# Kernel optimization log

Measured on AMD Instinct MI355X. Metric: run time of the kernel, lower is better.

Reference implementation:

```python
import jax, jax.numpy as jnp
import numpy as np

L = 1024  # seq_len


def setup_inputs() -> dict:
    key = jax.random.key(0)
    ks = jax.random.split(key, 9)
    B = 4
    x = jax.random.uniform(ks[0], (B, L, L), dtype=jnp.float32)          # scores from pre_model
    M = (jax.random.uniform(ks[1], (B, L, L)) < 0.5).astype(jnp.float32)  # pairing-constraint mask
    M = M * M.transpose(0, 2, 1)  # symmetric binary mask
    return {
        "x": x,
        "M": M,
        "s": jnp.float32(0.5),
        "w": jax.random.uniform(ks[2], (1,), dtype=jnp.float32),
        "rho_p": jax.random.uniform(ks[3], (L, L), dtype=jnp.float32),
        "alpha": jnp.float32(0.005),
        "belt": jnp.float32(0.05),
        "lr_alpha": jnp.float32(0.99),
        "lr_belt": jnp.float32(0.99),
        "steps": 16,
    }


def _T_A(A_hat, M):
    # symmetrize then mask
    return (A_hat + A_hat.transpose(0, 2, 1)) * 0.5 * M


def reference(x, M, s, w, rho_p, alpha, belt, lr_alpha, lr_belt, steps):
    scores = x                      # pre_model output, [B, L, L]
    U = scores - s
    A_hat0 = scores
    A0 = _T_A(A_hat0, M)
    Lm0 = w * jax.nn.relu(jnp.sum(A0, axis=-1) - 1.0)   # [B, L] (w broadcasts)

    def step(carry, t):
        Lm, A, A_hat = carry
        # G = U/2 - Lm * sign(rowsum(A) - 1), broadcast over last dim
        row = jnp.sum(A, axis=-1) - 1.0                  # [B, L]
        G = U * 0.5 - (Lm * jnp.sign(row))[:, :, None]   # [B, L, L]
        at = alpha * jnp.power(lr_alpha, t)
        A_hat = A_hat + at * A_hat * M * (G + G.transpose(0, 2, 1))
        A_hat = jax.nn.relu(jnp.abs(A_hat) - rho_p * at)  # soft threshold
        A_hat = 1.0 - jax.nn.relu(1.0 - A_hat)            # clip above at 1
        A = _T_A(A_hat, M)
        Lm = Lm + belt * jnp.power(lr_belt, t) * jax.nn.relu(jnp.sum(A, axis=-1) - 1.0)
        return (Lm, A, A_hat), None

    ts = jnp.arange(steps, dtype=jnp.float32)
    (Lm, A, A_hat), _ = jax.lax.scan(step, (Lm0, A0, A_hat0), ts)
    return A
```

## Files before the change

### kernel.cpp

```cpp
#include <hip/hip_runtime.h>
#include <cstddef>
#include <math.h>

static constexpr int L = 1024;
static constexpr int B = 4;
static constexpr int NSTEPS = 16;
static constexpr int NTILE = 16;
static constexpr int NPAIR = NTILE * (NTILE + 1) / 2;
static constexpr int BL = B * L;
static constexpr int NBLK = 256;
static constexpr int NBANK = 4;
static constexpr int NGRP = 16;
static constexpr int GBLK = NBLK / NGRP;

static constexpr size_t AH_OFF  = 0;
static constexpr size_t US_OFF  = (size_t)B * L * L;
static constexpr size_t CP_OFF  = 2 * (size_t)B * L * L;
static constexpr size_t RP0_OFF = CP_OFF + (size_t)B * 256 * L;
static constexpr size_t CP0_OFF = RP0_OFF + (size_t)B * 16 * L;
static constexpr size_t R_OFF   = CP0_OFF + (size_t)B * 16 * L;
static constexpr size_t LM_OFF  = R_OFF + (size_t)B * L;
static constexpr size_t CC_OFF  = LM_OFF + (size_t)B * L;
static constexpr size_t SC_OFF  = CC_OFF + (size_t)B * L;
static constexpr size_t RS_OFF  = SC_OFF + 64;
static constexpr size_t CS_OFF  = RS_OFF + (size_t)(NSTEPS - 1) * BL;
static constexpr size_t CS_U64  = (size_t)(NSTEPS - 1) * NBANK * BL;
static constexpr size_t BAR_OFF = CS_OFF + 2 * CS_U64;
static constexpr size_t NZERO_U64 = CS_U64 + 520;

__global__ __launch_bounds__(256) void init_kernel(
    const float* __restrict__ x, const float* __restrict__ M,
    const float* __restrict__ sp,
    float* __restrict__ ah, float* __restrict__ us,
    float* __restrict__ Rpart, float* __restrict__ Cpart0,
    unsigned long long* __restrict__ Cs)
{
    __shared__ float lt[64][65];
    __shared__ float cpw[4][64];
    const int bid  = blockIdx.x;
    {
        const size_t gid = (size_t)bid * 256 + threadIdx.x;
        if (gid < NZERO_U64) Cs[gid] = 0ull;
    }
    const int chunk = bid & 7;
    const int rest  = bid >> 3;
    const int b  = rest >> 5;
    const int ti = (chunk << 1) | ((rest >> 4) & 1);
    const int tj = rest & 15;
    const int t  = threadIdx.x;
    const int w  = t >> 6;
    const int r  = t >> 4;
    const int c4 = (t & 15) << 2;
    const float s = sp[0];
    const float* xb = x + (size_t)b * L * L;

#pragma unroll
    for (int it = 0; it < 4; ++it) {
        int rr = r + 16 * it;
        float4 v = *(const float4*)(xb + (size_t)(tj * 64 + rr) * L + ti * 64 + c4);
        lt[rr][c4+0] = v.x; lt[rr][c4+1] = v.y; lt[rr][c4+2] = v.z; lt[rr][c4+3] = v.w;
    }
    __syncthreads();

    float cs0 = 0.f, cs1 = 0.f, cs2 = 0.f, cs3 = 0.f;
#pragma unroll
    for (int it = 0; it < 4; ++it) {
        int rr = r + 16 * it;
        int gi = ti * 64 + rr;
        size_t off = (size_t)b * L * L + (size_t)gi * L + tj * 64 + c4;
        float4 xv = *(const float4*)(x + off);
        float4 mv = *(const float4*)(M + off);
        *(float4*)(us + off) = make_float4(0.5f*(xv.x + lt[c4+0][rr]) - s,
                                           0.5f*(xv.y + lt[c4+1][rr]) - s,
                                           0.5f*(xv.z + lt[c4+2][rr]) - s,
                                           0.5f*(xv.w + lt[c4+3][rr]) - s);
        float a0 = xv.x*mv.x, a1 = xv.y*mv.y, a2 = xv.z*mv.z, a3 = xv.w*mv.w;
        *(float4*)(ah + off) = make_float4(a0, a1, a2, a3);
        float rs = (a0 + a1) + (a2 + a3);
        rs += __shfl_xor(rs, 1); rs += __shfl_xor(rs, 2);
        rs += __shfl_xor(rs, 4); rs += __shfl_xor(rs, 8);
        if ((t & 15) == 0) Rpart[((size_t)(b * 16 + tj)) * L + gi] = rs;
        cs0 += a0; cs1 += a1; cs2 += a2; cs3 += a3;
    }
    cs0 += __shfl_xor(cs0, 16); cs0 += __shfl_xor(cs0, 32);
    cs1 += __shfl_xor(cs1, 16); cs1 += __shfl_xor(cs1, 32);
    cs2 += __shfl_xor(cs2, 16); cs2 += __shfl_xor(cs2, 32);
    cs3 += __shfl_xor(cs3, 16); cs3 += __shfl_xor(cs3, 32);
    if ((t & 63) < 16) {
        int c0 = (t & 63) << 2;
        cpw[w][c0+0] = cs0; cpw[w][c0+1] = cs1; cpw[w][c0+2] = cs2; cpw[w][c0+3] = cs3;
    }
    __syncthreads();
    if (t < 64)
        Cpart0[((size_t)(b * 16 + ti)) * L + tj * 64 + t] =
            (cpw[0][t] + cpw[1][t]) + (cpw[2][t] + cpw[3][t]);
}

__global__ __launch_bounds__(256) void lminit_kernel(
    const float* __restrict__ wp,
    const float* __restrict__ alphap, const float* __restrict__ beltp,
    const float* __restrict__ lrap,  const float* __restrict__ lrbp,
    const float* __restrict__ Rpart, const float* __restrict__ Cpart0,
    float* __restrict__ Lm, float* __restrict__ cc, float* __restrict__ sc)
{
    const int bid = blockIdx.x;
    const int t   = threadIdx.x;
    if (bid == 0 && t < NSTEPS) {
        sc[t]          = alphap[0] * powf(lrap[0], (float)t);
        sc[NSTEPS + t] = beltp[0]  * powf(lrbp[0], (float)t);
    }
    const int b   = bid >> 2;
    const int i   = ((bid & 3) << 8) + t;
    float R0 = 0.f, C0 = 0.f;
#pragma unroll
    for (int k = 0; k < 16; ++k) {
        R0 += Rpart[((size_t)(b * 16 + k)) * L + i];
        C0 += Cpart0[((size_t)(b * 16 + k)) * L + i];
    }
    float rowv = 0.5f * (R0 + C0) - 1.0f;
    float rl = fmaxf(rowv, 0.f);
    float lm = wp[0] * rl;
    Lm[b * L + i] = lm;
    float sg = (rowv > 0.f) ? 1.f : ((rowv < 0.f) ? -1.f : 0.f);
    cc[b * L + i] = lm * sg;
}

__device__ __forceinline__ float step_elem(float a, float u, float rho,
                                           float ci, float cj, float at) {
    float g = u - ci - cj;
    float v = a * (1.f + at * g);
    v = fmaxf(fabsf(v) - rho * at, 0.f);
    return fminf(v, 1.f);
}

__global__ __launch_bounds__(1024, 4) void steps_kernel(
    const float* __restrict__ rho, const float* __restrict__ sc,
    float* __restrict__ ah, const float* __restrict__ us,
    const float* __restrict__ Lm0, const float* __restrict__ cc0,
    float* __restrict__ Rs, unsigned long long* __restrict__ Cs,
    unsigned int* __restrict__ bar)
{
    __shared__ float cc_lds[1024];
    __shared__ float lm_lds[1024];
    __shared__ float cp[8][1024];

    const int t    = threadIdx.x;
    const int w    = t >> 6;
    const int l    = t & 63;
    const int bid  = blockIdx.x;
    const int xcd  = bid & 7;
    const int idx  = bid >> 3;
    const int b    = idx >> 3;
    const int slab = (xcd << 3) | (idx & 7);
    const int row  = (slab << 4) | w;
    const int bank = xcd & 3;
    const int grp  = bid >> 4;
    const size_t rowoff = (size_t)b * L * L + (size_t)row * L;
    const float* rrow = rho + (size_t)row * L;
    unsigned int* gctr = bar + grp * 64;
    unsigned int* root = bar + NGRP * 64;

    cc_lds[t] = cc0[b * L + t];
    lm_lds[t] = Lm0[b * L + t];

    float4 a4[4], u4[4];
#pragma unroll
    for (int k = 0; k < 4; ++k) {
        const size_t off = rowoff + (k << 8) + (l << 2);
        a4[k] = *(const float4*)(ah + off);
        u4[k] = *(const float4*)(us + off);
    }
    __syncthreads();

    for (int p = 0; p < NSTEPS; ++p) {
        const float at = sc[p];
        const float ci = cc_lds[row];
        float rs = 0.f;
#pragma unroll
        for (int k = 0; k < 4; ++k) {
            float4 h  = *(const float4*)(rrow + (k << 8) + (l << 2));
            float4 c4 = *(const float4*)&cc_lds[(k << 8) + (l << 2)];
            a4[k].x = step_elem(a4[k].x, u4[k].x, h.x, ci, c4.x, at);
            a4[k].y = step_elem(a4[k].y, u4[k].y, h.y, ci, c4.y, at);
            a4[k].z = step_elem(a4[k].z, u4[k].z, h.z, ci, c4.z, at);
            a4[k].w = step_elem(a4[k].w, u4[k].w, h.w, ci, c4.w, at);
            rs += (a4[k].x + a4[k].y) + (a4[k].z + a4[k].w);
        }
        if (p == NSTEPS - 1) break;

        rs += __shfl_xor(rs, 1);  rs += __shfl_xor(rs, 2);  rs += __shfl_xor(rs, 4);
        rs += __shfl_xor(rs, 8);  rs += __shfl_xor(rs, 16); rs += __shfl_xor(rs, 32);
        if (l == 0)
            __hip_atomic_store(&Rs[(size_t)p * BL + b * L + row], rs,
                               __ATOMIC_RELAXED, __HIP_MEMORY_SCOPE_AGENT);

        if (w >= 8) {
#pragma unroll
            for (int k = 0; k < 4; ++k)
                *(float4*)&cp[w - 8][(k << 8) + (l << 2)] = a4[k];
        }
        __syncthreads();
        if (w < 8) {
#pragma unroll
            for (int k = 0; k < 4; ++k) {
                float4* q = (float4*)&cp[w][(k << 8) + (l << 2)];
                float4 v = *q;
                v.x += a4[k].x; v.y += a4[k].y; v.z += a4[k].z; v.w += a4[k].w;
                *q = v;
            }
        }
        __syncthreads();
        float csum = 0.f;
#pragma unroll
        for (int j = 0; j < 8; ++j) csum += cp[j][t];
        atomicAdd(Cs + ((size_t)(p * NBANK + bank)) * BL + b * L + t,
                  (unsigned long long)((double)csum * 4294967296.0));

        __syncthreads();
        if (t == 0) {
            unsigned old = __hip_atomic_fetch_add(gctr, 1u, __ATOMIC_ACQ_REL,
                                                  __HIP_MEMORY_SCOPE_AGENT);
            if (old == (unsigned)(p * GBLK + GBLK - 1))
                __hip_atomic_fetch_add(root, 1u, __ATOMIC_ACQ_REL,
                                       __HIP_MEMORY_SCOPE_AGENT);
            const unsigned target = (unsigned)(p + 1) * (unsigned)NGRP;
            while (__hip_atomic_load(root, __ATOMIC_RELAXED,
                                     __HIP_MEMORY_SCOPE_AGENT) < target)
                __builtin_amdgcn_s_sleep(4);
            (void)__hip_atomic_load(root, __ATOMIC_ACQUIRE,
                                    __HIP_MEMORY_SCOPE_AGENT);
        }
        __syncthreads();

        {
            const size_t cbase = (size_t)p * NBANK * BL + b * L + t;
            unsigned long long craw = 0ull;
#pragma unroll
            for (int q = 0; q < NBANK; ++q)
                craw += __hip_atomic_load(&Cs[cbase + (size_t)q * BL],
                                          __ATOMIC_RELAXED, __HIP_MEMORY_SCOPE_AGENT);
            float Rv = __hip_atomic_load(
                &Rs[(size_t)p * BL + b * L + t],
                __ATOMIC_RELAXED, __HIP_MEMORY_SCOPE_AGENT);
            float Cv = (float)((double)(long long)craw * (1.0 / 4294967296.0));
            float rowv = 0.5f * (Rv + Cv) - 1.0f;
            float lm = lm_lds[t] + sc[NSTEPS + p] * fmaxf(rowv, 0.f);
            lm_lds[t] = lm;
            cc_lds[t] = lm * ((rowv > 0.f) ? 1.f : ((rowv < 0.f) ? -1.f : 0.f));
        }
        __syncthreads();
    }

#pragma unroll
    for (int k = 0; k < 4; ++k)
        *(float4*)(ah + rowoff + (k << 8) + (l << 2)) = a4[k];
}

template <bool DO_SUMS>
__global__ __launch_bounds__(512) void update_kernel(
    const float* __restrict__ rho, const float* __restrict__ sc,
    float* __restrict__ ah, const float* __restrict__ us,
    const float* __restrict__ cc,
    float* __restrict__ R, float* __restrict__ Cpart, int p)
{
    __shared__ float cp[8][1024];
    const int bid   = blockIdx.x;
    const int chunk = bid & 7;
    const int rest  = bid >> 3;
    const int b     = rest >> 4;
    const int slab  = (chunk << 4) | (rest & 15);
    const int t    = threadIdx.x;
    const int w    = t >> 6;
    const int l    = t & 63;
    const int row  = (slab << 3) + w;
    const size_t rowoff = (size_t)b * L * L + (size_t)row * L;
    const float at = sc[p];
    const float* ccb = cc + b * L;

    float4 cj[4];
#pragma unroll
    for (int k = 0; k < 4; ++k)
        cj[k] = *(const float4*)(ccb + k * 256 + l * 4);
    const float ci = ccb[row];

    float4 a4[4], u4[4], h4[4];
#pragma unroll
    for (int k = 0; k < 4; ++k) {
        const size_t off = rowoff + k * 256 + l * 4;
        a4[k] = *(const float4*)(ah + off);
        u4[k] = *(const float4*)(us + off);
        h4[k] = *(const float4*)(rho + (size_t)row * L + k * 256 + l * 4);
    }
#pragma unroll
    for (int k = 0; k < 4; ++k) {
        a4[k].x = step_elem(a4[k].x, u4[k].x, h4[k].x, ci, cj[k].x, at);
        a4[k].y = step_elem(a4[k].y, u4[k].y, h4[k].y, ci, cj[k].y, at);
        a4[k].z = step_elem(a4[k].z, u4[k].z, h4[k].z, ci, cj[k].z, at);
        a4[k].w = step_elem(a4[k].w, u4[k].w, h4[k].w, ci, cj[k].w, at);
        *(float4*)(ah + rowoff + k * 256 + l * 4) = a4[k];
    }

    if (DO_SUMS) {
        float rs = 0.f;
#pragma unroll
        for (int k = 0; k < 4; ++k)
            rs += (a4[k].x + a4[k].y) + (a4[k].z + a4[k].w);
        rs += __shfl_xor(rs, 1);  rs += __shfl_xor(rs, 2);  rs += __shfl_xor(rs, 4);
        rs += __shfl_xor(rs, 8);  rs += __shfl_xor(rs, 16); rs += __shfl_xor(rs, 32);
        if (l == 0) R[b * L + row] = rs;

#pragma unroll
        for (int k = 0; k < 4; ++k)
            *(float4*)&cp[w][k * 256 + l * 4] = a4[k];
        __syncthreads();
        const int c0 = t * 2;
        float2 acc = make_float2(0.f, 0.f);
#pragma unroll
        for (int j = 0; j < 8; ++j) {
            float2 v = *(float2*)&cp[j][c0];
            acc.x += v.x; acc.y += v.y;
        }
        *(float2*)(Cpart + ((size_t)(b * 128 + slab)) * L + c0) = acc;
    }
}

__global__ __launch_bounds__(1024) void lmreduce_kernel(
    const float* __restrict__ sc,
    const float* __restrict__ Cpart, const float* __restrict__ R,
    float* __restrict__ Lm, float* __restrict__ cc, int p)
{
    __shared__ float red[16][64];
    const int bid = blockIdx.x;
    const int b   = bid >> 4;
    const int c0  = (bid & 15) << 6;
    const int t   = threadIdx.x;
    const int w   = t >> 6;
    const int l   = t & 63;
    const int c   = c0 + l;

    const float* base = Cpart + (size_t)b * 128 * L + c;
    float v = 0.f;
#pragma unroll
    for (int k = w * 8; k < w * 8 + 8; ++k)
        v += base[(size_t)k * L];
    red[w][l] = v;
    __syncthreads();

    if (w == 0) {
        float total = 0.f;
#pragma unroll
        for (int j = 0; j < 16; ++j) total += red[j][l];
        float rowv = 0.5f * (R[b * L + c] + total) - 1.0f;
        float rl = fmaxf(rowv, 0.f);
        float lm = Lm[b * L + c] + sc[NSTEPS + p] * rl;
        Lm[b * L + c] = lm;
        float sg = (rowv > 0.f) ? 1.f : ((rowv < 0.f) ? -1.f : 0.f);
        cc[b * L + c] = lm * sg;
    }
}

__device__ __forceinline__ void decode_pair(int p, int& ti, int& tj) {
    int t = 0;
    while (p >= NTILE - t) { p -= NTILE - t; ++t; }
    ti = t; tj = t + p;
}

__global__ __launch_bounds__(256) void final_kernel(
    const float* __restrict__ ah, float* __restrict__ out)
{
    __shared__ float la[64][65];
    __shared__ float lb[64][65];
    const int task = blockIdx.x;
    const int b = task / NPAIR;
    int ti, tj; decode_pair(task % NPAIR, ti, tj);
    const int t  = threadIdx.x;
    const int r0 = t >> 4;
    const int c0 = (t & 15) << 2;
    const float* ahb = ah  + (size_t)b * L * L;
    float* ob        = out + (size_t)b * L * L;

    for (int it = 0; it < 4; ++it) {
        int r = r0 + 16 * it;
        float4 va = *(const float4*)(ahb + (size_t)(ti * 64 + r) * L + tj * 64 + c0);
        la[r][c0+0] = va.x; la[r][c0+1] = va.y; la[r][c0+2] = va.z; la[r][c0+3] = va.w;
        if (ti != tj) {
            float4 vb = *(const float4*)(ahb + (size_t)(tj * 64 + r) * L + ti * 64 + c0);
            lb[r][c0+0] = vb.x; lb[r][c0+1] = vb.y; lb[r][c0+2] = vb.z; lb[r][c0+3] = vb.w;
        }
    }
    __syncthreads();

    for (int it = 0; it < 4; ++it) {
        int r = r0 + 16 * it;
        size_t off = (size_t)(ti * 64 + r) * L + tj * 64 + c0;
        float tb0, tb1, tb2, tb3;
        if (ti == tj) { tb0 = la[c0+0][r]; tb1 = la[c0+1][r]; tb2 = la[c0+2][r]; tb3 = la[c0+3][r]; }
        else          { tb0 = lb[c0+0][r]; tb1 = lb[c0+1][r]; tb2 = lb[c0+2][r]; tb3 = lb[c0+3][r]; }
        *(float4*)(ob + off) = make_float4(0.5f*(la[r][c0+0]+tb0), 0.5f*(la[r][c0+1]+tb1),
                                           0.5f*(la[r][c0+2]+tb2), 0.5f*(la[r][c0+3]+tb3));
    }
    if (ti != tj) {
        for (int it = 0; it < 4; ++it) {
            int r = r0 + 16 * it;
            size_t off = (size_t)(tj * 64 + r) * L + ti * 64 + c0;
            *(float4*)(ob + off) = make_float4(0.5f*(lb[r][c0+0]+la[c0+0][r]),
                                               0.5f*(lb[r][c0+1]+la[c0+1][r]),
                                               0.5f*(lb[r][c0+2]+la[c0+2][r]),
                                               0.5f*(lb[r][c0+3]+la[c0+3][r]));
        }
    }
}

extern "C" void kernel_launch(void* const* d_in, const int* in_sizes, int n_in,
                              void* d_out, int out_size, void* d_ws, size_t ws_size,
                              hipStream_t stream) {
    const float* x     = (const float*)d_in[0];
    const float* M     = (const float*)d_in[1];
    const float* s     = (const float*)d_in[2];
    const float* w     = (const float*)d_in[3];
    const float* rho   = (const float*)d_in[4];
    const float* alpha = (const float*)d_in[5];
    const float* belt  = (const float*)d_in[6];
    const float* lra   = (const float*)d_in[7];
    const float* lrb   = (const float*)d_in[8];
    float* out = (float*)d_out;

    float* ws     = (float*)d_ws;
    float* ah     = ws + AH_OFF;
    float* us     = ws + US_OFF;
    float* Cpart  = ws + CP_OFF;
    float* Rpart  = ws + RP0_OFF;
    float* Cpart0 = ws + CP0_OFF;
    float* R      = ws + R_OFF;
    float* Lm     = ws + LM_OFF;
    float* cc     = ws + CC_OFF;
    float* sc     = ws + SC_OFF;
    float* Rs     = ws + RS_OFF;
    unsigned long long* Cs = (unsigned long long*)(ws + CS_OFF);
    unsigned int* bar      = (unsigned int*)(ws + BAR_OFF);

    init_kernel<<<dim3(1024), dim3(256), 0, stream>>>(x, M, s, ah, us, Rpart, Cpart0, Cs);
    lminit_kernel<<<dim3(16), dim3(256), 0, stream>>>(
        w, alpha, belt, lra, lrb, Rpart, Cpart0, Lm, cc, sc);

    {
        const float* rho_ = rho; const float* sc_ = sc;
        float* ah_ = ah; const float* us_ = us;
        const float* Lm_ = Lm; const float* cc_ = cc;
        float* Rs_ = Rs; unsigned long long* Cs_ = Cs;
        unsigned int* bar_ = bar;
        void* args[] = { &rho_, &sc_, &ah_, &us_, &Lm_, &cc_, &Rs_, &Cs_, &bar_ };
        hipError_t err = hipLaunchCooperativeKernel(
            (void*)steps_kernel, dim3(NBLK), dim3(1024), args, 0, stream);
        if (err != hipSuccess) {
            for (int p = 0; p < NSTEPS; ++p) {
                if (p < NSTEPS - 1) {
                    update_kernel<true><<<dim3(512), dim3(512), 0, stream>>>(
                        rho, sc, ah, us, cc, R, Cpart, p);
                    lmreduce_kernel<<<dim3(64), dim3(1024), 0, stream>>>(
                        sc, Cpart, R, Lm, cc, p);
                } else {
                    update_kernel<false><<<dim3(512), dim3(512), 0, stream>>>(
                        rho, sc, ah, us, cc, R, Cpart, p);
                }
            }
        }
    }

    final_kernel<<<dim3(B * NPAIR), dim3(256), 0, stream>>>(ah, out);
}
```

Measured before the change: 317.5 us.

## Scope grid barrier per batch and fold row sums into column atomics

Replaces the global two-level barrier with an independent barrier per batch (8 XCD groups of 8 blocks each), since each batch's Lagrange update only depends on its own sums. Row sums are added into the same fixed-point atomic accumulator as column sums (pre-scaled by 0.5), removing the separate Rs buffer and its load. rho and step scalars are cached in registers/LDS once instead of reloaded each step, and the spin sleep is shortened. Increases register pressure and atomic traffic to the accumulator slots.

```diff
diff --git a/kernel.cpp b/kernel.cpp
--- a/kernel.cpp
+++ b/kernel.cpp
@@ -10,8 +10,6 @@
 static constexpr int BL = B * L;
 static constexpr int NBLK = 256;
 static constexpr int NBANK = 4;
-static constexpr int NGRP = 16;
-static constexpr int GBLK = NBLK / NGRP;
 
 static constexpr size_t AH_OFF  = 0;
 static constexpr size_t US_OFF  = (size_t)B * L * L;
@@ -26,7 +24,7 @@
 static constexpr size_t CS_OFF  = RS_OFF + (size_t)(NSTEPS - 1) * BL;
 static constexpr size_t CS_U64  = (size_t)(NSTEPS - 1) * NBANK * BL;
 static constexpr size_t BAR_OFF = CS_OFF + 2 * CS_U64;
-static constexpr size_t NZERO_U64 = CS_U64 + 520;
+static constexpr size_t NZERO_U64 = CS_U64 + 576;
 
 __global__ __launch_bounds__(256) void init_kernel(
     const float* __restrict__ x, const float* __restrict__ M,
@@ -137,11 +135,12 @@
     const float* __restrict__ rho, const float* __restrict__ sc,
     float* __restrict__ ah, const float* __restrict__ us,
     const float* __restrict__ Lm0, const float* __restrict__ cc0,
-    float* __restrict__ Rs, unsigned long long* __restrict__ Cs,
+    unsigned long long* __restrict__ Cs,
     unsigned int* __restrict__ bar)
 {
     __shared__ float cc_lds[1024];
     __shared__ float lm_lds[1024];
+    __shared__ float sc_lds[2 * NSTEPS];
     __shared__ float cp[8][1024];
 
     const int t    = threadIdx.x;
@@ -153,46 +152,47 @@
     const int b    = idx >> 3;
     const int slab = (xcd << 3) | (idx & 7);
     const int row  = (slab << 4) | w;
-    const int bank = xcd & 3;
-    const int grp  = bid >> 4;
+    const int bank = xcd & (NBANK - 1);
     const size_t rowoff = (size_t)b * L * L + (size_t)row * L;
-    const float* rrow = rho + (size_t)row * L;
-    unsigned int* gctr = bar + grp * 64;
-    unsigned int* root = bar + NGRP * 64;
+    unsigned int* gctr = bar + ((b << 3) | xcd) * 32;
+    unsigned int* root = bar + 1024 + b * 32;
 
     cc_lds[t] = cc0[b * L + t];
     lm_lds[t] = Lm0[b * L + t];
-
-    float4 a4[4], u4[4];
+    if (t < 2 * NSTEPS) sc_lds[t] = sc[t];
+
+    float4 a4[4], u4[4], h4[4];
 #pragma unroll
     for (int k = 0; k < 4; ++k) {
         const size_t off = rowoff + (k << 8) + (l << 2);
         a4[k] = *(const float4*)(ah + off);
         u4[k] = *(const float4*)(us + off);
+        h4[k] = *(const float4*)(rho + (size_t)row * L + (k << 8) + (l << 2));
     }
     __syncthreads();
 
     for (int p = 0; p < NSTEPS; ++p) {
-        const float at = sc[p];
+        const float at = sc_lds[p];
         const float ci = cc_lds[row];
         float rs = 0.f;
 #pragma unroll
         for (int k = 0; k < 4; ++k) {
-            float4 h  = *(const float4*)(rrow + (k << 8) + (l << 2));
             float4 c4 = *(const float4*)&cc_lds[(k << 8) + (l << 2)];
-            a4[k].x = step_elem(a4[k].x, u4[k].x, h.x, ci, c4.x, at);
-            a4[k].y = step_elem(a4[k].y, u4[k].y, h.y, ci, c4.y, at);
-            a4[k].z = step_elem(a4[k].z, u4[k].z, h.z, ci, c4.z, at);
-            a4[k].w = step_elem(a4[k].w, u4[k].w, h.w, ci, c4.w, at);
+            a4[k].x = step_elem(a4[k].x, u4[k].x, h4[k].x, ci, c4.x, at);
+            a4[k].y = step_elem(a4[k].y, u4[k].y, h4[k].y, ci, c4.y, at);
+            a4[k].z = step_elem(a4[k].z, u4[k].z, h4[k].z, ci, c4.z, at);
+            a4[k].w = step_elem(a4[k].w, u4[k].w, h4[k].w, ci, c4.w, at);
             rs += (a4[k].x + a4[k].y) + (a4[k].z + a4[k].w);
         }
         if (p == NSTEPS - 1) break;
+
+        const size_t cslice = ((size_t)(p * NBANK + bank)) * BL + b * L;
 
         rs += __shfl_xor(rs, 1);  rs += __shfl_xor(rs, 2);  rs += __shfl_xor(rs, 4);
         rs += __shfl_xor(rs, 8);  rs += __shfl_xor(rs, 16); rs += __shfl_xor(rs, 32);
         if (l == 0)
-            __hip_atomic_store(&Rs[(size_t)p * BL + b * L + row], rs,
-                               __ATOMIC_RELAXED, __HIP_MEMORY_SCOPE_AGENT);
+            atomicAdd(Cs + cslice + row,
+                      (unsigned long long)((double)(0.5f * rs) * 4294967296.0));
 
         if (w >= 8) {
 #pragma unroll
@@ -213,20 +213,20 @@
         float csum = 0.f;
 #pragma unroll
         for (int j = 0; j < 8; ++j) csum += cp[j][t];
-        atomicAdd(Cs + ((size_t)(p * NBANK + bank)) * BL + b * L + t,
-                  (unsigned long long)((double)csum * 4294967296.0));
+        atomicAdd(Cs + cslice + t,
+                  (unsigned long long)((double)(0.5f * csum) * 4294967296.0));
 
         __syncthreads();
         if (t == 0) {
             unsigned old = __hip_atomic_fetch_add(gctr, 1u, __ATOMIC_ACQ_REL,
                                                   __HIP_MEMORY_SCOPE_AGENT);
-            if (old == (unsigned)(p * GBLK + GBLK - 1))
+            if (old == (unsigned)(p * 8 + 7))
                 __hip_atomic_fetch_add(root, 1u, __ATOMIC_ACQ_REL,
                                        __HIP_MEMORY_SCOPE_AGENT);
-            const unsigned target = (unsigned)(p + 1) * (unsigned)NGRP;
+            const unsigned target = (unsigned)(p + 1) * 8u;
             while (__hip_atomic_load(root, __ATOMIC_RELAXED,
                                      __HIP_MEMORY_SCOPE_AGENT) < target)
-                __builtin_amdgcn_s_sleep(4);
+                __builtin_amdgcn_s_sleep(1);
             (void)__hip_atomic_load(root, __ATOMIC_ACQUIRE,
                                     __HIP_MEMORY_SCOPE_AGENT);
         }
@@ -239,12 +239,8 @@
             for (int q = 0; q < NBANK; ++q)
                 craw += __hip_atomic_load(&Cs[cbase + (size_t)q * BL],
                                           __ATOMIC_RELAXED, __HIP_MEMORY_SCOPE_AGENT);
-            float Rv = __hip_atomic_load(
-                &Rs[(size_t)p * BL + b * L + t],
-                __ATOMIC_RELAXED, __HIP_MEMORY_SCOPE_AGENT);
-            float Cv = (float)((double)(long long)craw * (1.0 / 4294967296.0));
-            float rowv = 0.5f * (Rv + Cv) - 1.0f;
-            float lm = lm_lds[t] + sc[NSTEPS + p] * fmaxf(rowv, 0.f);
+            float rowv = (float)((double)craw * (1.0 / 4294967296.0)) - 1.0f;
+            float lm = lm_lds[t] + sc_lds[NSTEPS + p] * fmaxf(rowv, 0.f);
             lm_lds[t] = lm;
             cc_lds[t] = lm * ((rowv > 0.f) ? 1.f : ((rowv < 0.f) ? -1.f : 0.f));
         }
@@ -435,7 +431,6 @@
     float* Lm     = ws + LM_OFF;
     float* cc     = ws + CC_OFF;
     float* sc     = ws + SC_OFF;
-    float* Rs     = ws + RS_OFF;
     unsigned long long* Cs = (unsigned long long*)(ws + CS_OFF);
     unsigned int* bar      = (unsigned int*)(ws + BAR_OFF);
 
@@ -447,9 +442,9 @@
         const float* rho_ = rho; const float* sc_ = sc;
         float* ah_ = ah; const float* us_ = us;
         const float* Lm_ = Lm; const float* cc_ = cc;
-        float* Rs_ = Rs; unsigned long long* Cs_ = Cs;
+        unsigned long long* Cs_ = Cs;
         unsigned int* bar_ = bar;
-        void* args[] = { &rho_, &sc_, &ah_, &us_, &Lm_, &cc_, &Rs_, &Cs_, &bar_ };
+        void* args[] = { &rho_, &sc_, &ah_, &us_, &Lm_, &cc_, &Cs_, &bar_ };
         hipError_t err = hipLaunchCooperativeKernel(
             (void*)steps_kernel, dim3(NBLK), dim3(1024), args, 0, stream);
         if (err != hipSuccess) {
```

New measurement: 288.8 us. 9.0% less time.
